# Kernel tuning notes

Measured on AMD Instinct MI355X. Metric: run time of the kernel, lower is better.

Reference implementation:

```python
import jax, jax.numpy as jnp
import numpy as np

DIM = 1024
NUM_HEADS = 16
HEAD_DIM = DIM // NUM_HEADS
SCALE = HEAD_DIM ** -0.5


def setup_inputs() -> dict:
    key = jax.random.key(0)
    k_x, k_qkv, k_pw, k_pb = jax.random.split(key, 4)
    B, S = 2, 2048
    x = jax.random.normal(k_x, (B, S, DIM), dtype=jnp.float32)
    # nn.Linear(dim, 3*dim, bias=False): weight [3*dim, dim]
    w_qkv = jax.random.normal(k_qkv, (3 * DIM, DIM), dtype=jnp.float32) * (DIM ** -0.5)
    # nn.Linear(dim, dim): weight [dim, dim], bias [dim]
    w_proj = jax.random.normal(k_pw, (DIM, DIM), dtype=jnp.float32) * (DIM ** -0.5)
    b_proj = jax.random.normal(k_pb, (DIM,), dtype=jnp.float32) * 0.01
    return {"x": x, "w_qkv": w_qkv, "w_proj": w_proj, "b_proj": b_proj}


def reference(x, w_qkv, w_proj, b_proj):
    B, S, D = x.shape
    qkv = jnp.einsum("bsd,ed->bse", x, w_qkv)  # [B,S,3D]
    q, k, v = jnp.split(qkv, 3, axis=-1)
    def heads(t):  # [B,S,D] -> [B,H,S,hd]
        return t.reshape(B, S, NUM_HEADS, HEAD_DIM).transpose(0, 2, 1, 3)
    q, k, v = heads(q), heads(k), heads(v)
    attn = jnp.einsum("bhqd,bhkd->bhqk", q, k) * SCALE  # [B,H,S,S]
    attn = jax.nn.softmax(attn, axis=-1)
    out = jnp.einsum("bhqk,bhkd->bhqd", attn, v)  # [B,H,S,hd]
    out = out.transpose(0, 2, 1, 3).reshape(B, S, D)
    return jnp.einsum("bsd,ed->bse", out, w_proj) + b_proj
```

## Files before the change

### kernel.cpp

```cpp
#include <hip/hip_runtime.h>
#include <stdint.h>

typedef __bf16 bf16;
typedef __bf16 bf16x8 __attribute__((ext_vector_type(8)));
typedef float f32x4 __attribute__((ext_vector_type(4)));
typedef float f32x16 __attribute__((ext_vector_type(16)));

typedef __attribute__((address_space(1))) void gvoid_t;
typedef __attribute__((address_space(3))) void lvoid_t;

__device__ __forceinline__ void gload16(const void* src, void* lds) {
    __builtin_amdgcn_global_load_lds((gvoid_t*)src, (lvoid_t*)lds, 16, 0, 0);
}

__global__ __launch_bounds__(256) void cvt_kernel(const float* __restrict__ in,
                                                  bf16* __restrict__ out, int n8) {
    int idx = blockIdx.x * 256 + threadIdx.x;
    int stride = gridDim.x * 256;
    for (int i = idx; i < n8; i += stride) {
        const float4* p = (const float4*)in;
        float4 a = p[(long)i * 2], b = p[(long)i * 2 + 1];
        bf16x8 o;
        o[0] = (bf16)a.x; o[1] = (bf16)a.y; o[2] = (bf16)a.z; o[3] = (bf16)a.w;
        o[4] = (bf16)b.x; o[5] = (bf16)b.y; o[6] = (bf16)b.z; o[7] = (bf16)b.w;
        ((bf16x8*)out)[i] = o;
    }
}

template <bool F32OUT, int BN>
__global__ __launch_bounds__(256) void gemm_bt(const bf16* __restrict__ A,
                                               const bf16* __restrict__ W,
                                               const float* __restrict__ bias,
                                               void* __restrict__ Cout,
                                               const int M, const int N, const int K) {
    constexpr int NT = BN / 32;
    __shared__ __align__(16) bf16 Alds[4096];
    __shared__ __align__(16) bf16 Blds[4096];
    const int t = threadIdx.x;
    const int wid = t >> 6, lane = t & 63;
    const int g = lane >> 4, c = lane & 15;
    const int wm = wid >> 1, wn = wid & 1;
    const long bm = (long)blockIdx.y * 128, bn = (long)blockIdx.x * BN;

    f32x4 acc[4][NT] = {};

    const int arow = t >> 2;
    const int acol = (t & 3) * 8;
    const bf16* Asrc = A + (bm + arow) * (long)K + acol;
    const bf16* Bsrc = W + (bn + arow) * (long)K + acol;
    bf16* adst = Alds + wid * 512;
    bf16* bdst = Blds + wid * 512;

    for (int k0 = 0; k0 < K; k0 += 32) {
        gload16(Asrc + k0, adst);
        gload16(Asrc + k0 + (long)64 * K, adst + 2048);
        gload16(Bsrc + k0, bdst);
        if constexpr (BN == 128)
            gload16(Bsrc + k0 + (long)64 * K, bdst + 2048);
        __syncthreads();
        bf16x8 af[4], bfr[NT];
#pragma unroll
        for (int mt = 0; mt < 4; ++mt)
            af[mt] = *(const bf16x8*)(Alds + (wm * 64 + mt * 16 + c) * 32 + g * 8);
#pragma unroll
        for (int nt = 0; nt < NT; ++nt)
            bfr[nt] = *(const bf16x8*)(Blds + (wn * (BN / 2) + nt * 16 + c) * 32 + g * 8);
#pragma unroll
        for (int mt = 0; mt < 4; ++mt)
#pragma unroll
            for (int nt = 0; nt < NT; ++nt)
                acc[mt][nt] = __builtin_amdgcn_mfma_f32_16x16x32_bf16(af[mt], bfr[nt],
                                                                      acc[mt][nt], 0, 0, 0);
        __syncthreads();
    }
#pragma unroll
    for (int mt = 0; mt < 4; ++mt) {
#pragma unroll
        for (int nt = 0; nt < NT; ++nt) {
#pragma unroll
            for (int i = 0; i < 4; ++i) {
                const long row = bm + wm * 64 + mt * 16 + g * 4 + i;
                const long col = bn + wn * (BN / 2) + nt * 16 + c;
                if constexpr (F32OUT) {
                    ((float*)Cout)[row * N + col] = acc[mt][nt][i] + bias[col];
                } else {
                    ((bf16*)Cout)[row * N + col] = (bf16)acc[mt][nt][i];
                }
            }
        }
    }
}

__global__ __launch_bounds__(256) void vtrans_kernel(const bf16* __restrict__ qkv,
                                                     bf16* __restrict__ Vt) {
    __shared__ float Lf[64 * 65];
    const int t = threadIdx.x;
    const int bid = blockIdx.x;
    const int b = bid >> 9, r = bid & 511;
    const int s0 = (r & 31) * 64, hd0 = (r >> 5) * 64;

    const int sr = t >> 3, scol = (t & 7) * 8;
    const bf16* src = qkv + (long)(b * 2048 + s0 + sr) * 3072 + 2048 + hd0 + scol;
    bf16x8 v0 = *(const bf16x8*)src;
    bf16x8 v1 = *(const bf16x8*)(src + (long)32 * 3072);
#pragma unroll
    for (int e = 0; e < 8; ++e) {
        Lf[(scol + e) * 65 + sr] = (float)v0[e];
        Lf[(scol + e) * 65 + sr + 32] = (float)v1[e];
    }
    __syncthreads();
    const int hr = t >> 2, ss = (t & 3) * 16;
    bf16 outv[16];
#pragma unroll
    for (int j = 0; j < 16; ++j) outv[j] = (bf16)Lf[hr * 65 + ss + j];
    bf16* dst = Vt + ((long)b * 1024 + hd0 + hr) * 2048 + s0 + ss;
    *(bf16x8*)dst = *(bf16x8*)outv;
    *(bf16x8*)(dst + 8) = *(bf16x8*)(outv + 8);
}

__global__ __launch_bounds__(256) void flash_kernel(const bf16* __restrict__ qkv,
                                                    const bf16* __restrict__ Vt,
                                                    bf16* __restrict__ attno) {
    __shared__ __align__(16) bf16 KV[16384];
    __shared__ float LP[128];

    const int t = threadIdx.x;
    const int wid = t >> 6, lane = t & 63;
    const int l31 = lane & 31, hl = lane >> 5;

    const int i0 = blockIdx.x;
    const int xcd = i0 & 7, slot = i0 >> 3;
    const int bh = xcd * 4 + (slot >> 4);
    const int qb = slot & 15;
    const int b = bh >> 4, h = bh & 15;
    const int rowbase = b * 2048;
    const int q0w = qb * 128 + wid * 32;

    bf16x8 qf[4];
    {
        const bf16* qrow = qkv + (long)(rowbase + q0w + l31) * 3072 + h * 64 + hl * 8;
        const float qs = 0.18033688f;
#pragma unroll
        for (int ks = 0; ks < 4; ++ks) {
            bf16x8 a = *(const bf16x8*)(qrow + ks * 16);
#pragma unroll
            for (int e = 0; e < 8; ++e) qf[ks][e] = (bf16)((float)a[e] * qs);
        }
    }

    const int srow = t >> 3, sq = t & 7;
    const int swcol = (sq ^ (srow & 7)) * 8;
    const bf16* ksrc = qkv + (long)(rowbase + srow) * 3072 + 1024 + h * 64 + swcol;
    const bf16* vsrc = Vt + ((long)b * 1024 + h * 64 + srow) * 2048 + swcol;
    bf16* kdst = KV + wid * 512;
    bf16* vdst = KV + 8192 + wid * 512;

    int rdoff[4];
#pragma unroll
    for (int ks = 0; ks < 4; ++ks)
        rdoff[ks] = l31 * 64 + (((ks * 2 + hl) ^ (l31 & 7)) * 8);

    float lpart = 0.f;
    f32x16 oacc0 = {}, oacc1 = {};

    gload16(ksrc, kdst);
    gload16(ksrc + (long)32 * 3072, kdst + 2048);
    gload16(vsrc, vdst);
    gload16(vsrc + 32 * 2048, vdst + 2048);
    __syncthreads();

    for (int tt = 0; tt < 32; ++tt) {
        const int bi = tt & 1;
        if (tt < 31) {
            const long kadd = (long)(tt + 1) * 64 * 3072;
            const int vadd = (tt + 1) * 64;
            const int obi = bi ^ 1;
            gload16(ksrc + kadd, kdst + obi * 4096);
            gload16(ksrc + kadd + (long)32 * 3072, kdst + obi * 4096 + 2048);
            gload16(vsrc + vadd, vdst + obi * 4096);
            gload16(vsrc + vadd + 32 * 2048, vdst + obi * 4096 + 2048);
        }
        const bf16* Kb = KV + bi * 4096;
        const bf16* Vb = KV + 8192 + bi * 4096;

        f32x16 s0 = {}, s1 = {};
#pragma unroll
        for (int ks = 0; ks < 4; ++ks) {
            bf16x8 kf0 = *(const bf16x8*)(Kb + rdoff[ks]);
            bf16x8 kf1 = *(const bf16x8*)(Kb + 2048 + rdoff[ks]);
            s0 = __builtin_amdgcn_mfma_f32_32x32x16_bf16(kf0, qf[ks], s0, 0, 0, 0);
            s1 = __builtin_amdgcn_mfma_f32_32x32x16_bf16(kf1, qf[ks], s1, 0, 0, 0);
        }

        float p0[16], p1[16];
#pragma unroll
        for (int r = 0; r < 16; ++r) { p0[r] = exp2f(s0[r]); lpart += p0[r]; }
#pragma unroll
        for (int r = 0; r < 16; ++r) { p1[r] = exp2f(s1[r]); lpart += p1[r]; }

#pragma unroll
        for (int ks = 0; ks < 4; ++ks) {
            const float* pp = (ks < 2) ? p0 : p1;
            const int s = (ks & 1) * 8;
            unsigned wA, wB, wC, wD;
            asm("v_cvt_pk_bf16_f32 %0, %1, %2" : "=v"(wA) : "v"(pp[s + 0]), "v"(pp[s + 1]));
            asm("v_cvt_pk_bf16_f32 %0, %1, %2" : "=v"(wB) : "v"(pp[s + 4]), "v"(pp[s + 5]));
            asm("v_cvt_pk_bf16_f32 %0, %1, %2" : "=v"(wC) : "v"(pp[s + 2]), "v"(pp[s + 3]));
            asm("v_cvt_pk_bf16_f32 %0, %1, %2" : "=v"(wD) : "v"(pp[s + 6]), "v"(pp[s + 7]));
            asm("v_permlane32_swap_b32 %0, %1" : "+v"(wA), "+v"(wB));
            asm("v_permlane32_swap_b32 %0, %1" : "+v"(wC), "+v"(wD));
            union { unsigned w[4]; bf16x8 v; } pu;
            pu.w[0] = wA; pu.w[1] = wC; pu.w[2] = wB; pu.w[3] = wD;
            bf16x8 vf0 = *(const bf16x8*)(Vb + rdoff[ks]);
            bf16x8 vf1 = *(const bf16x8*)(Vb + 2048 + rdoff[ks]);
            oacc0 = __builtin_amdgcn_mfma_f32_32x32x16_bf16(pu.v, vf0, oacc0, 0, 0, 0);
            oacc1 = __builtin_amdgcn_mfma_f32_32x32x16_bf16(pu.v, vf1, oacc1, 0, 0, 0);
        }
        __syncthreads();
    }

    lpart += __shfl_xor(lpart, 32);
    if (lane < 32) LP[wid * 32 + l31] = lpart;
    float inv[16];
#pragma unroll
    for (int r = 0; r < 16; ++r) {
        const int qrow = (r & 3) + 8 * (r >> 2) + 4 * hl;
        inv[r] = 1.0f / LP[wid * 32 + qrow];
    }

#pragma unroll
    for (int r = 0; r < 16; ++r) {
        const int qrow = (r & 3) + 8 * (r >> 2) + 4 * hl;
        const long rbase = (long)(rowbase + q0w + qrow) * 1024 + h * 64 + l31;
        attno[rbase] = (bf16)(oacc0[r] * inv[r]);
        attno[rbase + 32] = (bf16)(oacc1[r] * inv[r]);
    }
}

extern "C" void kernel_launch(void* const* d_in, const int* in_sizes, int n_in,
                              void* d_out, int out_size, void* d_ws, size_t ws_size,
                              hipStream_t stream) {
    const float* x = (const float*)d_in[0];
    const float* wqkv = (const float*)d_in[1];
    const float* wproj = (const float*)d_in[2];
    const float* bproj = (const float*)d_in[3];

    char* ws = (char*)d_ws;
    bf16* xb     = (bf16*)(ws);
    bf16* Vt     = (bf16*)(ws);
    bf16* wqkvb  = (bf16*)(ws + 8388608);
    bf16* wprojb = (bf16*)(ws + 14680064);
    bf16* qkv    = (bf16*)(ws + 16777216);
    bf16* attno  = (bf16*)(ws + 41943040);
    if (ws_size < 50331648) return;

    cvt_kernel<<<2048, 256, 0, stream>>>(x, xb, 524288);
    cvt_kernel<<<1536, 256, 0, stream>>>(wqkv, wqkvb, 393216);
    cvt_kernel<<<512, 256, 0, stream>>>(wproj, wprojb, 131072);

    gemm_bt<false, 128><<<dim3(24, 32), 256, 0, stream>>>(xb, wqkvb, nullptr, qkv,
                                                          4096, 3072, 1024);

    vtrans_kernel<<<1024, 256, 0, stream>>>(qkv, Vt);

    flash_kernel<<<512, 256, 0, stream>>>(qkv, Vt, attno);

    gemm_bt<true, 64><<<dim3(16, 32), 256, 0, stream>>>(attno, wprojb, bproj, d_out,
                                                        4096, 1024, 1024);
}
```

Before: 145.7 us.

## Triple-buffer K/V tiles in flash kernel with vmcnt waits and raw exp

Moves the flash attention K/V staging from a double buffer with a full __syncthreads per iteration to a three-slot LDS ring. A manual s_waitcnt vmcnt(4) plus s_barrier lets the next tile's global-to-LDS loads stay in flight while the current tile is computed. It also swaps exp2f for a raw v_exp_f32 and splits the row-sum accumulation into four independent partial sums to shorten the dependency chain. LDS use grows from 32KB to 48KB per block, which may lower occupancy, and the hand-counted vmcnt values and unguarded raw exp need to be right for correctness.

New measurement: 129.1 us. -11.4%, faster.

```diff
diff --git a/kernel.cpp b/kernel.cpp
--- a/kernel.cpp
+++ b/kernel.cpp
@@ -11,6 +11,12 @@
 
 __device__ __forceinline__ void gload16(const void* src, void* lds) {
     __builtin_amdgcn_global_load_lds((gvoid_t*)src, (lvoid_t*)lds, 16, 0, 0);
+}
+
+__device__ __forceinline__ float fexp2(float x) {
+    float r;
+    asm("v_exp_f32 %0, %1" : "=v"(r) : "v"(x));
+    return r;
 }
 
 __global__ __launch_bounds__(256) void cvt_kernel(const float* __restrict__ in,
@@ -121,7 +127,7 @@
 __global__ __launch_bounds__(256) void flash_kernel(const bf16* __restrict__ qkv,
                                                     const bf16* __restrict__ Vt,
                                                     bf16* __restrict__ attno) {
-    __shared__ __align__(16) bf16 KV[16384];
+    __shared__ __align__(16) bf16 KV[24576];
     __shared__ float LP[128];
 
     const int t = threadIdx.x;
@@ -150,39 +156,36 @@
 
     const int srow = t >> 3, sq = t & 7;
     const int swcol = (sq ^ (srow & 7)) * 8;
-    const bf16* ksrc = qkv + (long)(rowbase + srow) * 3072 + 1024 + h * 64 + swcol;
-    const bf16* vsrc = Vt + ((long)b * 1024 + h * 64 + srow) * 2048 + swcol;
-    bf16* kdst = KV + wid * 512;
-    bf16* vdst = KV + 8192 + wid * 512;
+    const bf16* ksn = qkv + (long)(rowbase + srow) * 3072 + 1024 + h * 64 + swcol;
+    const bf16* vsn = Vt + ((long)b * 1024 + h * 64 + srow) * 2048 + swcol;
 
     int rdoff[4];
 #pragma unroll
     for (int ks = 0; ks < 4; ++ks)
         rdoff[ks] = l31 * 64 + (((ks * 2 + hl) ^ (l31 & 7)) * 8);
 
-    float lpart = 0.f;
+    float lpA = 0.f, lpB = 0.f, lpC = 0.f, lpD = 0.f;
     f32x16 oacc0 = {}, oacc1 = {};
 
-    gload16(ksrc, kdst);
-    gload16(ksrc + (long)32 * 3072, kdst + 2048);
-    gload16(vsrc, vdst);
-    gload16(vsrc + 32 * 2048, vdst + 2048);
-    __syncthreads();
-
-    for (int tt = 0; tt < 32; ++tt) {
-        const int bi = tt & 1;
-        if (tt < 31) {
-            const long kadd = (long)(tt + 1) * 64 * 3072;
-            const int vadd = (tt + 1) * 64;
-            const int obi = bi ^ 1;
-            gload16(ksrc + kadd, kdst + obi * 4096);
-            gload16(ksrc + kadd + (long)32 * 3072, kdst + obi * 4096 + 2048);
-            gload16(vsrc + vadd, vdst + obi * 4096);
-            gload16(vsrc + vadd + 32 * 2048, vdst + obi * 4096 + 2048);
-        }
+    auto stage = [&]() __attribute__((always_inline)) {
+    };
+    (void)stage;
+
+#define STAGE(BI)                                                        \
+    {                                                                    \
+        bf16* kd = KV + (BI) * 4096 + wid * 512;                         \
+        bf16* vd = KV + 12288 + (BI) * 4096 + wid * 512;                 \
+        gload16(ksn, kd);                                                \
+        gload16(ksn + 98304, kd + 2048);                                 \
+        gload16(vsn, vd);                                                \
+        gload16(vsn + 65536, vd + 2048);                                 \
+        ksn += 196608;                                                   \
+        vsn += 64;                                                       \
+    }
+
+    auto compute = [&](int bi) __attribute__((always_inline)) {
         const bf16* Kb = KV + bi * 4096;
-        const bf16* Vb = KV + 8192 + bi * 4096;
-
+        const bf16* Vb = KV + 12288 + bi * 4096;
         f32x16 s0 = {}, s1 = {};
 #pragma unroll
         for (int ks = 0; ks < 4; ++ks) {
@@ -191,13 +194,18 @@
             s0 = __builtin_amdgcn_mfma_f32_32x32x16_bf16(kf0, qf[ks], s0, 0, 0, 0);
             s1 = __builtin_amdgcn_mfma_f32_32x32x16_bf16(kf1, qf[ks], s1, 0, 0, 0);
         }
-
         float p0[16], p1[16];
 #pragma unroll
-        for (int r = 0; r < 16; ++r) { p0[r] = exp2f(s0[r]); lpart += p0[r]; }
-#pragma unroll
-        for (int r = 0; r < 16; ++r) { p1[r] = exp2f(s1[r]); lpart += p1[r]; }
-
+        for (int r = 0; r < 16; ++r) p0[r] = fexp2(s0[r]);
+#pragma unroll
+        for (int r = 0; r < 16; ++r) p1[r] = fexp2(s1[r]);
+#pragma unroll
+        for (int r = 0; r < 4; ++r) {
+            lpA += p0[r * 4 + 0] + p1[r * 4 + 0];
+            lpB += p0[r * 4 + 1] + p1[r * 4 + 1];
+            lpC += p0[r * 4 + 2] + p1[r * 4 + 2];
+            lpD += p0[r * 4 + 3] + p1[r * 4 + 3];
+        }
 #pragma unroll
         for (int ks = 0; ks < 4; ++ks) {
             const float* pp = (ks < 2) ? p0 : p1;
@@ -216,9 +224,32 @@
             oacc0 = __builtin_amdgcn_mfma_f32_32x32x16_bf16(pu.v, vf0, oacc0, 0, 0, 0);
             oacc1 = __builtin_amdgcn_mfma_f32_32x32x16_bf16(pu.v, vf1, oacc1, 0, 0, 0);
         }
-        __syncthreads();
-    }
-
+    };
+
+    STAGE(0);
+    STAGE(1);
+
+#define FSTEP(CUR, NXT)                                    \
+    asm volatile("s_waitcnt vmcnt(4)" ::: "memory");       \
+    __builtin_amdgcn_s_barrier();                          \
+    STAGE(NXT);                                            \
+    compute(CUR);
+
+    for (int t3 = 0; t3 < 10; ++t3) {
+        FSTEP(0, 2)
+        FSTEP(1, 0)
+        FSTEP(2, 1)
+    }
+    asm volatile("s_waitcnt vmcnt(4)" ::: "memory");
+    __builtin_amdgcn_s_barrier();
+    compute(0);
+    asm volatile("s_waitcnt vmcnt(0)" ::: "memory");
+    __builtin_amdgcn_s_barrier();
+    compute(1);
+#undef FSTEP
+#undef STAGE
+
+    float lpart = (lpA + lpB) + (lpC + lpD);
     lpart += __shfl_xor(lpart, 32);
     if (lane < 32) LP[wid * 32 + l31] = lpart;
     float inv[16];
```
